# Performance work log

Hardware: AMD Instinct MI355X
Metric: run time of the kernel (lower is better)

The kernel has to match this reference:

```python
import jax, jax.numpy as jnp
import numpy as np
import math

B, L, D, H = 4, 2048, 1024, 16
DK = D // H


def setup_inputs() -> dict:
    key = jax.random.key(0)
    ks = jax.random.split(key, 12)
    scale = math.sqrt(6.0 / (D + D))  # xavier_uniform for square Linear
    def lin(k):
        return jax.random.uniform(k, (D, D), jnp.float32, -scale, scale)
    inp = {
        "query": jax.random.normal(ks[0], (B, L, D), jnp.float32),
        "key": jax.random.normal(ks[1], (B, L, D), jnp.float32),
        "value": jax.random.normal(ks[2], (B, L, D), jnp.float32),
        "Wq": lin(ks[3]), "bq": jnp.zeros((D,), jnp.float32),
        "Wk": lin(ks[4]), "bk": jnp.zeros((D,), jnp.float32),
        "Wv": lin(ks[5]), "bv": jnp.zeros((D,), jnp.float32),
        "Wo": lin(ks[6]), "bo": jnp.zeros((D,), jnp.float32),
        # causal mask: True means masked (hide future positions)
        "attn_mask": jnp.triu(jnp.ones((L, L), dtype=bool), k=1),
    }
    return inp


def reference(query, key, value, Wq, bq, Wk, bk, Wv, bv, Wo, bo, attn_mask):
    def proj(x, W, b):
        # torch Linear: x @ W.T + b ; then split heads -> [B, H, L, DK]
        y = jnp.einsum('bld,ed->ble', x, W) + b
        return y.reshape(B, L, H, DK).transpose(0, 2, 1, 3)

    q = proj(query, Wq, bq)
    k = proj(key, Wk, bk)
    v = proj(value, Wv, bv)

    scores = jnp.einsum('bhqd,bhkd->bhqk', q, k) / jnp.sqrt(jnp.float32(DK))
    scores = jnp.where(attn_mask[None, None, :, :], jnp.float32(-jnp.inf), scores)
    p_attn = jax.nn.softmax(scores, axis=-1)  # dropout p=0 (eval)

    ctx = jnp.einsum('bhqk,bhkd->bhqd', p_attn, v)
    ctx = ctx.transpose(0, 2, 1, 3).reshape(B, L, D)
    out = jnp.einsum('bld,ed->ble', ctx, Wo) + bo
    return out
```

## Files before the change

kernel.cpp:

```cpp
#include <hip/hip_runtime.h>
#include <hip/hip_bf16.h>
#include <stdint.h>

typedef unsigned short u16;
typedef unsigned int u32;
typedef short short8 __attribute__((ext_vector_type(8)));
typedef float f32x4 __attribute__((ext_vector_type(4)));
typedef u32 u32x4 __attribute__((ext_vector_type(4)));
typedef u32 u32x2 __attribute__((ext_vector_type(2)));

#define DEV static __device__ __forceinline__

constexpr int Bsz = 4, Lseq = 2048, Dm = 1024, Hn = 16, Dk = 64;
constexpr float LOG2E = 1.44269504088896340736f;
constexpr float QSCALE = 0.125f * LOG2E;

DEV u16 f2bf(float x) {
    u32 u = __builtin_bit_cast(u32, x);
    return (u16)((u + 0x7fffu + ((u >> 16) & 1u)) >> 16);
}

DEV u32 pk2(float a, float b) {
    __hip_bfloat162 h = __float22bfloat162_rn(float2{a, b});
    u32 r;
    __builtin_memcpy(&r, &h, 4);
    return r;
}

DEV u32x4 ld8_cvt(const float* p) {
    f32x4 lo = *(const f32x4*)p;
    f32x4 hi = *(const f32x4*)(p + 4);
    u32x4 r;
    r[0] = pk2(lo[0], lo[1]);
    r[1] = pk2(lo[2], lo[3]);
    r[2] = pk2(hi[0], hi[1]);
    r[3] = pk2(hi[2], hi[3]);
    return r;
}

DEV void glds16(const void* g, void* l) {
    __builtin_amdgcn_global_load_lds(
        (const __attribute__((address_space(1))) void*)g,
        (__attribute__((address_space(3))) void*)l, 16, 0, 0);
}

__global__ __launch_bounds__(256) void cvt_w3(
    const float* __restrict__ a, const float* __restrict__ b,
    const float* __restrict__ c, u16* __restrict__ d, int n8)
{
    int i = blockIdx.x * 256 + threadIdx.x;
    if (i >= n8) return;
    const float* s = blockIdx.y == 0 ? a : (blockIdx.y == 1 ? b : c);
    ((u32x4*)(d + (size_t)blockIdx.y * (size_t)n8 * 8))[i] = ld8_cvt(s + (long)i * 8);
}

__global__ __launch_bounds__(256) void gemm_oproj(
    const u16* __restrict__ A, const float* __restrict__ W,
    const float* __restrict__ bias, float* __restrict__ Cout)
{
    __shared__ u16 At[2][128 * 32];
    __shared__ u16 Bt[2][128 * 32];

    const int tid = threadIdx.x;
    const int lane = tid & 63, wid = tid >> 6;
    const int wr = wid >> 1, wc = wid & 1;
    const int mbase = blockIdx.x * 128, nbase = blockIdx.y * 128;

    f32x4 acc[4][4];
#pragma unroll
    for (int i = 0; i < 4; i++)
#pragma unroll
        for (int j = 0; j < 4; j++) acc[i][j] = (f32x4)0.f;

    const int srow = lane >> 2;
    const int sseg = (lane & 3) * 8;
    auto stageA = [&](int kt, int buf) {
#pragma unroll
        for (int c = 0; c < 2; c++) {
            const int sec = wid * 2 + c;
            glds16(A + (long)(mbase + sec * 16 + srow) * Dm + (long)kt * 32 + sseg,
                   &At[buf][sec * 512]);
        }
    };

    u32x4 vb[2];
    auto loadB = [&](int kt) {
#pragma unroll
        for (int i = 0; i < 2; i++) {
            int idx = i * 256 + tid;
            int row = idx >> 2, seg = idx & 3;
            vb[i] = ld8_cvt(W + (long)(nbase + row) * Dm + (long)kt * 32 + seg * 8);
        }
    };
    auto writeB = [&](int buf) {
#pragma unroll
        for (int i = 0; i < 2; i++) {
            int idx = i * 256 + tid;
            *(u32x4*)&Bt[buf][idx * 8] = vb[i];
        }
    };

    stageA(0, 0);
    loadB(0);
    writeB(0);
    __syncthreads();

    for (int kt = 0; kt < 32; kt++) {
        const int cur = kt & 1;
        const bool more = (kt + 1 < 32);
        if (more) {
            stageA(kt + 1, cur ^ 1);
            loadB(kt + 1);
        }
        short8 af[4], bfr[4];
#pragma unroll
        for (int mf = 0; mf < 4; mf++)
            af[mf] = *(const short8*)&At[cur][(wr * 64 + mf * 16 + (lane & 15)) * 32 + (lane >> 4) * 8];
#pragma unroll
        for (int nf = 0; nf < 4; nf++)
            bfr[nf] = *(const short8*)&Bt[cur][(wc * 64 + nf * 16 + (lane & 15)) * 32 + (lane >> 4) * 8];
        __builtin_amdgcn_s_setprio(1);
#pragma unroll
        for (int mf = 0; mf < 4; mf++)
#pragma unroll
            for (int nf = 0; nf < 4; nf++)
                acc[mf][nf] = __builtin_amdgcn_mfma_f32_16x16x32_bf16(af[mf], bfr[nf], acc[mf][nf], 0, 0, 0);
        __builtin_amdgcn_s_setprio(0);
        if (more) writeB(cur ^ 1);
        __syncthreads();
    }

#pragma unroll
    for (int nf = 0; nf < 4; nf++) {
        const int n = nbase + wc * 64 + nf * 16 + (lane & 15);
        const float bv = bias[n];
#pragma unroll
        for (int mf = 0; mf < 4; mf++) {
            const int m0 = mbase + wr * 64 + mf * 16 + (lane >> 4) * 4;
#pragma unroll
            for (int r = 0; r < 4; r++) {
                const int m = m0 + r;
                Cout[(long)m * Dm + n] = acc[mf][nf][r] + bv;
            }
        }
    }
}

__global__ __launch_bounds__(256) void gemm_qkv(
    const float* __restrict__ Xq, const float* __restrict__ Xk,
    const float* __restrict__ Xv, const u16* __restrict__ Wb3,
    const float* __restrict__ bq, const float* __restrict__ bk,
    const float* __restrict__ bv, u16* __restrict__ Out3)
{
    __shared__ u16 At[2][128 * 32];
    __shared__ u16 Bt[2][128 * 32];

    const int tid = threadIdx.x;
    const int lane = tid & 63, wid = tid >> 6;
    const int wr = wid >> 1, wc = wid & 1;
    const int mbase = blockIdx.x * 128;
    const int t = blockIdx.y >> 3;
    const int nbase = (blockIdx.y & 7) * 128;
    const float* X = t == 0 ? Xq : (t == 1 ? Xk : Xv);
    const u16* Bw = Wb3 + (size_t)t * Dm * Dm;
    const float* bias = t == 0 ? bq : (t == 1 ? bk : bv);
    const float scale = t == 0 ? QSCALE : 1.0f;
    u16* Cout = Out3 + (size_t)t * ((size_t)Bsz * Lseq * Dm);

    f32x4 acc[4][4];
#pragma unroll
    for (int i = 0; i < 4; i++)
#pragma unroll
        for (int j = 0; j < 4; j++) acc[i][j] = (f32x4)0.f;

    const int srow = lane >> 2;
    const int sseg = (lane & 3) * 8;
    auto stageB = [&](int kt, int buf) {
#pragma unroll
        for (int c = 0; c < 2; c++) {
            const int sec = wid * 2 + c;
            glds16(Bw + (long)(nbase + sec * 16 + srow) * Dm + (long)kt * 32 + sseg,
                   &Bt[buf][sec * 512]);
        }
    };

    u32x4 va[2];
    auto loadA = [&](int kt) {
#pragma unroll
        for (int i = 0; i < 2; i++) {
            int idx = i * 256 + tid;
            int row = idx >> 2, seg = idx & 3;
            va[i] = ld8_cvt(X + (long)(mbase + row) * Dm + (long)kt * 32 + seg * 8);
        }
    };
    auto writeA = [&](int buf) {
#pragma unroll
        for (int i = 0; i < 2; i++) {
            int idx = i * 256 + tid;
            *(u32x4*)&At[buf][idx * 8] = va[i];
        }
    };

    stageB(0, 0);
    loadA(0);
    writeA(0);
    __syncthreads();

    for (int kt = 0; kt < 32; kt++) {
        const int cur = kt & 1;
        const bool more = (kt + 1 < 32);
        if (more) {
            stageB(kt + 1, cur ^ 1);
            loadA(kt + 1);
        }
        short8 af[4], bfr[4];
#pragma unroll
        for (int mf = 0; mf < 4; mf++)
            af[mf] = *(const short8*)&At[cur][(wr * 64 + mf * 16 + (lane & 15)) * 32 + (lane >> 4) * 8];
#pragma unroll
        for (int nf = 0; nf < 4; nf++)
            bfr[nf] = *(const short8*)&Bt[cur][(wc * 64 + nf * 16 + (lane & 15)) * 32 + (lane >> 4) * 8];
        __builtin_amdgcn_s_setprio(1);
#pragma unroll
        for (int mf = 0; mf < 4; mf++)
#pragma unroll
            for (int nf = 0; nf < 4; nf++)
                acc[mf][nf] = __builtin_amdgcn_mfma_f32_16x16x32_bf16(af[mf], bfr[nf], acc[mf][nf], 0, 0, 0);
        __builtin_amdgcn_s_setprio(0);
        if (more) writeA(cur ^ 1);
        __syncthreads();
    }

#pragma unroll
    for (int nf = 0; nf < 4; nf++) {
        const int n = nbase + wc * 64 + nf * 16 + (lane & 15);
        const float bv = bias[n];
#pragma unroll
        for (int mf = 0; mf < 4; mf++) {
            const int m0 = mbase + wr * 64 + mf * 16 + (lane >> 4) * 4;
#pragma unroll
            for (int r = 0; r < 4; r++) {
                const int m = m0 + r;
                const float v = (acc[mf][nf][r] + bv) * scale;
                int b = m >> 11, l = m & 2047, h = n >> 6, dk = n & 63;
                long addr = ((long)(b * Hn + h) * Lseq + l) * Dk + dk;
                Cout[addr] = f2bf(v);
            }
        }
    }
}

__global__ __launch_bounds__(256) void attn_fwd(
    const u16* __restrict__ Qb, const u16* __restrict__ Kb,
    const u16* __restrict__ Vb, u16* __restrict__ Ctx)
{
    __shared__ u16 Kt[2][64 * 64];
    __shared__ u16 Vt[2][64 * 64];
    __shared__ u16 Pq[4][32 * 64];

    const int tid = threadIdx.x, lane = tid & 63, w = tid >> 6;
    const int qt = gridDim.y - 1 - blockIdx.y;
    const int bh = blockIdx.x;
    const long base = (long)bh * Lseq * Dk;
    const int qw = qt * 128 + w * 32;

    const int krow_in_w = lane >> 3;
    const int kseg = lane & 7;
    const int vp = tid >> 3;
    const int vd0 = (tid & 7) * 8;

    auto stage_k = [&](int kvbase, int buf) {
#pragma unroll
        for (int c = 0; c < 2; c++) {
            int kv = w * 16 + c * 8 + krow_in_w;
            int d0 = ((kseg ^ (kv & 7)) * 8);
            glds16(Kb + base + (long)(kvbase + kv) * Dk + d0,
                   &Kt[buf][(w * 16 + c * 8) * 64]);
        }
    };

    auto write_v = [&](int buf, const u32x4& r0, const u32x4& r1) {
        const u16* p0 = (const u16*)&r0;
        const u16* p1 = (const u16*)&r1;
#pragma unroll
        for (int j = 0; j < 8; j++) {
            int d = vd0 + j;
            u32 pr = (u32)p0[j] | ((u32)p1[j] << 16);
            int kvx = (2 * vp) ^ ((((d & 7) ^ (d >> 3)) & 7) << 3);
            *(u32*)&Vt[buf][d * 64 + kvx] = pr;
        }
    };

    short8 qfr[2][2];
#pragma unroll
    for (int qf = 0; qf < 2; qf++)
#pragma unroll
        for (int ks = 0; ks < 2; ks++) {
            int q = qw + qf * 16 + (lane & 15);
            int d0 = ks * 32 + (lane >> 4) * 8;
            qfr[qf][ks] = *(const short8*)(Qb + base + (long)q * Dk + d0);
        }

    f32x4 accT[4][2];
#pragma unroll
    for (int i = 0; i < 4; i++)
#pragma unroll
        for (int j = 0; j < 2; j++) accT[i][j] = (f32x4)0.f;
    float m_run[2] = {-__builtin_inff(), -__builtin_inff()};
    float l_part[2] = {0.f, 0.f};

    u32x4 vr0, vr1;
    stage_k(0, 0);
    vr0 = *(const u32x4*)(Vb + base + (long)(2 * vp) * Dk + vd0);
    vr1 = *(const u32x4*)(Vb + base + (long)(2 * vp + 1) * Dk + vd0);
    write_v(0, vr0, vr1);
    __syncthreads();

    const int nkv = qt * 2 + 2;
    const int myn = ((qw + 31) >> 6) + 1;

    for (int kvt = 0; kvt < nkv; kvt++) {
        const int cur = kvt & 1;
        const bool more = (kvt + 1 < nkv);
        const int kvbase = kvt * 64;

        if (more) {
            stage_k(kvbase + 64, cur ^ 1);
            vr0 = *(const u32x4*)(Vb + base + (long)(kvbase + 64 + 2 * vp) * Dk + vd0);
            vr1 = *(const u32x4*)(Vb + base + (long)(kvbase + 64 + 2 * vp + 1) * Dk + vd0);
        }

        if (kvt < myn) {
            f32x4 st[4][2];
#pragma unroll
            for (int i = 0; i < 4; i++)
#pragma unroll
                for (int j = 0; j < 2; j++) st[i][j] = (f32x4)0.f;
            __builtin_amdgcn_s_setprio(1);
#pragma unroll
            for (int ks = 0; ks < 2; ks++) {
                short8 kf[4];
#pragma unroll
                for (int kvf = 0; kvf < 4; kvf++) {
                    int row = kvf * 16 + (lane & 15);
                    int d0 = ks * 32 + (lane >> 4) * 8;
                    kf[kvf] = *(const short8*)&Kt[cur][row * 64 + (d0 ^ ((row & 7) << 3))];
                }
#pragma unroll
                for (int kvf = 0; kvf < 4; kvf++)
#pragma unroll
                    for (int qf = 0; qf < 2; qf++)
                        st[kvf][qf] = __builtin_amdgcn_mfma_f32_16x16x32_bf16(kf[kvf], qfr[qf][ks], st[kvf][qf], 0, 0, 0);
            }
            __builtin_amdgcn_s_setprio(0);

            if ((kvbase + 63) > qw) {
#pragma unroll
                for (int qf = 0; qf < 2; qf++) {
                    const int q = qw + qf * 16 + (lane & 15);
#pragma unroll
                    for (int kvf = 0; kvf < 4; kvf++)
#pragma unroll
                        for (int r = 0; r < 4; r++) {
                            int kv = kvbase + kvf * 16 + (lane >> 4) * 4 + r;
                            if (kv > q) st[kvf][qf][r] = -1e30f;
                        }
                }
            }

#pragma unroll
            for (int qf = 0; qf < 2; qf++) {
                float tmax = st[0][qf][0];
#pragma unroll
                for (int kvf = 0; kvf < 4; kvf++)
#pragma unroll
                    for (int r = 0; r < 4; r++) tmax = fmaxf(tmax, st[kvf][qf][r]);
                tmax = fmaxf(tmax, __shfl_xor(tmax, 16, 64));
                tmax = fmaxf(tmax, __shfl_xor(tmax, 32, 64));
                const bool norescale = __all((int)(tmax <= m_run[qf] + 8.f));
                if (!norescale) {
                    const float mnew = fmaxf(m_run[qf], tmax);
                    const float sc = __builtin_exp2f(m_run[qf] - mnew);
                    m_run[qf] = mnew;
                    l_part[qf] *= sc;
#pragma unroll
                    for (int dkf = 0; dkf < 4; dkf++)
#pragma unroll
                        for (int r = 0; r < 4; r++) accT[dkf][qf][r] *= sc;
                }
                const float mq = m_run[qf];
                float ts = 0.f;
#pragma unroll
                for (int kvf = 0; kvf < 4; kvf++)
#pragma unroll
                    for (int r = 0; r < 4; r++) {
                        float p = __builtin_exp2f(st[kvf][qf][r] - mq);
                        st[kvf][qf][r] = p;
                        ts += p;
                    }
                l_part[qf] += ts;
                const int qrow = qf * 16 + (lane & 15);
#pragma unroll
                for (int kvf = 0; kvf < 4; kvf++) {
                    u32x2 pk;
                    pk[0] = pk2(st[kvf][qf][0], st[kvf][qf][1]);
                    pk[1] = pk2(st[kvf][qf][2], st[kvf][qf][3]);
                    int kvi = (kvf * 16 + (lane >> 4) * 4) ^ ((lane & 7) << 3);
                    *(u32x2*)&Pq[w][qrow * 64 + kvi] = pk;
                }
            }

#pragma unroll
            for (int kf2 = 0; kf2 < 2; kf2++) {
                short8 vfr[4];
#pragma unroll
                for (int dkf = 0; dkf < 4; dkf++) {
                    int d = dkf * 16 + (lane & 15);
                    int kvi = (kf2 * 32 + (lane >> 4) * 8) ^ ((((d & 7) ^ (d >> 3)) & 7) << 3);
                    vfr[dkf] = *(const short8*)&Vt[cur][d * 64 + kvi];
                }
                short8 pfr[2];
#pragma unroll
                for (int qf = 0; qf < 2; qf++) {
                    int qrow = qf * 16 + (lane & 15);
                    int kvi = (kf2 * 32 + (lane >> 4) * 8) ^ ((lane & 7) << 3);
                    pfr[qf] = *(const short8*)&Pq[w][qrow * 64 + kvi];
                }
                __builtin_amdgcn_s_setprio(1);
#pragma unroll
                for (int dkf = 0; dkf < 4; dkf++)
#pragma unroll
                    for (int qf = 0; qf < 2; qf++)
                        accT[dkf][qf] = __builtin_amdgcn_mfma_f32_16x16x32_bf16(vfr[dkf], pfr[qf], accT[dkf][qf], 0, 0, 0);
                __builtin_amdgcn_s_setprio(0);
            }
        }

        if (more) write_v(cur ^ 1, vr0, vr1);
        __syncthreads();
    }

    const int b = bh >> 4, h = bh & 15;
#pragma unroll
    for (int qf = 0; qf < 2; qf++) {
        float l = l_part[qf];
        l += __shfl_xor(l, 16, 64);
        l += __shfl_xor(l, 32, 64);
        const float inv = 1.f / l;
        const int q = qw + qf * 16 + (lane & 15);
#pragma unroll
        for (int dkf = 0; dkf < 4; dkf++) {
            const int dk0 = dkf * 16 + (lane >> 4) * 4;
            u32x2 o;
            o[0] = pk2(accT[dkf][qf][0] * inv, accT[dkf][qf][1] * inv);
            o[1] = pk2(accT[dkf][qf][2] * inv, accT[dkf][qf][3] * inv);
            long addr = ((long)b * Lseq + q) * Dm + h * Dk + dk0;
            *(u32x2*)(Ctx + addr) = o;
        }
    }
}

extern "C" void kernel_launch(void* const* d_in, const int* in_sizes, int n_in,
                              void* d_out, int out_size, void* d_ws, size_t ws_size,
                              hipStream_t stream)
{
    const float* query = (const float*)d_in[0];
    const float* key_  = (const float*)d_in[1];
    const float* value = (const float*)d_in[2];
    const float* Wq = (const float*)d_in[3];
    const float* bq = (const float*)d_in[4];
    const float* Wk = (const float*)d_in[5];
    const float* bk = (const float*)d_in[6];
    const float* Wv = (const float*)d_in[7];
    const float* bv = (const float*)d_in[8];
    const float* Wo = (const float*)d_in[9];
    const float* bo = (const float*)d_in[10];

    float* out = (float*)d_out;
    const size_t tens = (size_t)Bsz * Lseq * Dm;
    const size_t wTot = (size_t)Dm * Dm;
    u16* Qb = (u16*)d_ws;
    u16* Kb = Qb + tens;
    u16* Vb = Kb + tens;
    u16* Cx = Vb + tens;
    u16* Wqb = Cx;

    dim3 blk(256), g(64, 8), gq(64, 24);
    const int n8w = (int)(wTot / 8);
    const int gw = (n8w + 255) / 256;

    cvt_w3<<<dim3(gw, 3), blk, 0, stream>>>(Wq, Wk, Wv, Wqb, n8w);
    gemm_qkv<<<gq, blk, 0, stream>>>(query, key_, value, Wqb, bq, bk, bv, Qb);
    attn_fwd<<<dim3(Bsz * Hn, Lseq / 128), blk, 0, stream>>>(Qb, Kb, Vb, Cx);
    gemm_oproj<<<g, blk, 0, stream>>>(Cx, Wo, bo, out);
}
```

Before: 212.9 us.

## Switch attention to 32x32x16 MFMA and pass P through registers via permlane swap

The attention kernel moves from 16x16x32 MFMA tiles to 32x32x16 tiles, so each lane owns one query column. The softmax then reduces with a single cross-half shuffle. The probability tile no longer round-trips through shared memory: it is packed to bf16 and rearranged with v_permlane32_swap into the B-operand layout for the PV MFMA. This removes the Pq LDS buffer and its writes and reads, but uses larger accumulator vectors, which raises register pressure and relies on a gfx950-specific instruction.

```diff
diff --git a/kernel.cpp b/kernel.cpp
--- a/kernel.cpp
+++ b/kernel.cpp
@@ -6,6 +6,7 @@
 typedef unsigned int u32;
 typedef short short8 __attribute__((ext_vector_type(8)));
 typedef float f32x4 __attribute__((ext_vector_type(4)));
+typedef float f32x16 __attribute__((ext_vector_type(16)));
 typedef u32 u32x4 __attribute__((ext_vector_type(4)));
 typedef u32 u32x2 __attribute__((ext_vector_type(2)));
 
@@ -42,6 +43,18 @@
     __builtin_amdgcn_global_load_lds(
         (const __attribute__((address_space(1))) void*)g,
         (__attribute__((address_space(3))) void*)l, 16, 0, 0);
+}
+
+DEV void pswap(u32& a, u32& b) {
+    asm volatile("v_permlane32_swap_b32 %0, %1" : "+v"(a), "+v"(b));
+}
+
+DEV short8 mk8(u32 w0, u32 w1, u32 w2, u32 w3) {
+    u32x4 t;
+    t[0] = w0; t[1] = w1; t[2] = w2; t[3] = w3;
+    short8 r;
+    __builtin_memcpy(&r, &t, 16);
+    return r;
 }
 
 __global__ __launch_bounds__(256) void cvt_w3(
@@ -256,13 +269,13 @@
 {
     __shared__ u16 Kt[2][64 * 64];
     __shared__ u16 Vt[2][64 * 64];
-    __shared__ u16 Pq[4][32 * 64];
 
     const int tid = threadIdx.x, lane = tid & 63, w = tid >> 6;
     const int qt = gridDim.y - 1 - blockIdx.y;
     const int bh = blockIdx.x;
     const long base = (long)bh * Lseq * Dk;
     const int qw = qt * 128 + w * 32;
+    const int qcol = lane & 31, hi = lane >> 5;
 
     const int krow_in_w = lane >> 3;
     const int kseg = lane & 7;
@@ -291,23 +304,14 @@
         }
     };
 
-    short8 qfr[2][2];
-#pragma unroll
-    for (int qf = 0; qf < 2; qf++)
-#pragma unroll
-        for (int ks = 0; ks < 2; ks++) {
-            int q = qw + qf * 16 + (lane & 15);
-            int d0 = ks * 32 + (lane >> 4) * 8;
-            qfr[qf][ks] = *(const short8*)(Qb + base + (long)q * Dk + d0);
-        }
-
-    f32x4 accT[4][2];
-#pragma unroll
-    for (int i = 0; i < 4; i++)
-#pragma unroll
-        for (int j = 0; j < 2; j++) accT[i][j] = (f32x4)0.f;
-    float m_run[2] = {-__builtin_inff(), -__builtin_inff()};
-    float l_part[2] = {0.f, 0.f};
+    short8 qfr[4];
+#pragma unroll
+    for (int ks = 0; ks < 4; ks++)
+        qfr[ks] = *(const short8*)(Qb + base + (long)(qw + qcol) * Dk + ks * 16 + hi * 8);
+
+    f32x16 acc0 = (f32x16)0.f, acc1 = (f32x16)0.f;
+    float m_run = -__builtin_inff();
+    float l_part = 0.f;
 
     u32x4 vr0, vr1;
     stage_k(0, 0);
@@ -331,131 +335,136 @@
         }
 
         if (kvt < myn) {
-            f32x4 st[4][2];
-#pragma unroll
-            for (int i = 0; i < 4; i++)
-#pragma unroll
-                for (int j = 0; j < 2; j++) st[i][j] = (f32x4)0.f;
+            f32x16 st0 = (f32x16)0.f, st1 = (f32x16)0.f;
             __builtin_amdgcn_s_setprio(1);
 #pragma unroll
-            for (int ks = 0; ks < 2; ks++) {
-                short8 kf[4];
-#pragma unroll
-                for (int kvf = 0; kvf < 4; kvf++) {
-                    int row = kvf * 16 + (lane & 15);
-                    int d0 = ks * 32 + (lane >> 4) * 8;
-                    kf[kvf] = *(const short8*)&Kt[cur][row * 64 + (d0 ^ ((row & 7) << 3))];
+            for (int ks = 0; ks < 4; ks++) {
+                const int d0 = ks * 16 + hi * 8;
+                {
+                    const int kvrow = qcol;
+                    short8 kf = *(const short8*)&Kt[cur][kvrow * 64 + (d0 ^ ((kvrow & 7) << 3))];
+                    st0 = __builtin_amdgcn_mfma_f32_32x32x16_bf16(kf, qfr[ks], st0, 0, 0, 0);
                 }
-#pragma unroll
-                for (int kvf = 0; kvf < 4; kvf++)
-#pragma unroll
-                    for (int qf = 0; qf < 2; qf++)
-                        st[kvf][qf] = __builtin_amdgcn_mfma_f32_16x16x32_bf16(kf[kvf], qfr[qf][ks], st[kvf][qf], 0, 0, 0);
+                {
+                    const int kvrow = 32 + qcol;
+                    short8 kf = *(const short8*)&Kt[cur][kvrow * 64 + (d0 ^ ((kvrow & 7) << 3))];
+                    st1 = __builtin_amdgcn_mfma_f32_32x32x16_bf16(kf, qfr[ks], st1, 0, 0, 0);
+                }
             }
             __builtin_amdgcn_s_setprio(0);
 
             if ((kvbase + 63) > qw) {
-#pragma unroll
-                for (int qf = 0; qf < 2; qf++) {
-                    const int q = qw + qf * 16 + (lane & 15);
-#pragma unroll
-                    for (int kvf = 0; kvf < 4; kvf++)
-#pragma unroll
-                        for (int r = 0; r < 4; r++) {
-                            int kv = kvbase + kvf * 16 + (lane >> 4) * 4 + r;
-                            if (kv > q) st[kvf][qf][r] = -1e30f;
-                        }
+                const int q = qw + qcol;
+#pragma unroll
+                for (int r = 0; r < 16; r++) {
+                    const int rr = (r & 3) + 8 * (r >> 2) + 4 * hi;
+                    if (kvbase + rr > q) st0[r] = -1e30f;
+                    if (kvbase + 32 + rr > q) st1[r] = -1e30f;
                 }
             }
 
-#pragma unroll
-            for (int qf = 0; qf < 2; qf++) {
-                float tmax = st[0][qf][0];
-#pragma unroll
-                for (int kvf = 0; kvf < 4; kvf++)
-#pragma unroll
-                    for (int r = 0; r < 4; r++) tmax = fmaxf(tmax, st[kvf][qf][r]);
-                tmax = fmaxf(tmax, __shfl_xor(tmax, 16, 64));
-                tmax = fmaxf(tmax, __shfl_xor(tmax, 32, 64));
-                const bool norescale = __all((int)(tmax <= m_run[qf] + 8.f));
-                if (!norescale) {
-                    const float mnew = fmaxf(m_run[qf], tmax);
-                    const float sc = __builtin_exp2f(m_run[qf] - mnew);
-                    m_run[qf] = mnew;
-                    l_part[qf] *= sc;
-#pragma unroll
-                    for (int dkf = 0; dkf < 4; dkf++)
-#pragma unroll
-                        for (int r = 0; r < 4; r++) accT[dkf][qf][r] *= sc;
+            float tmax = st0[0];
+#pragma unroll
+            for (int r = 1; r < 16; r++) tmax = fmaxf(tmax, st0[r]);
+#pragma unroll
+            for (int r = 0; r < 16; r++) tmax = fmaxf(tmax, st1[r]);
+            tmax = fmaxf(tmax, __shfl_xor(tmax, 32, 64));
+            const bool norescale = __all((int)(tmax <= m_run + 8.f));
+            if (!norescale) {
+                const float mnew = fmaxf(m_run, tmax);
+                const float sc = __builtin_exp2f(m_run - mnew);
+                m_run = mnew;
+                l_part *= sc;
+#pragma unroll
+                for (int r = 0; r < 16; r++) {
+                    acc0[r] *= sc;
+                    acc1[r] *= sc;
                 }
-                const float mq = m_run[qf];
-                float ts = 0.f;
-#pragma unroll
-                for (int kvf = 0; kvf < 4; kvf++)
-#pragma unroll
-                    for (int r = 0; r < 4; r++) {
-                        float p = __builtin_exp2f(st[kvf][qf][r] - mq);
-                        st[kvf][qf][r] = p;
-                        ts += p;
-                    }
-                l_part[qf] += ts;
-                const int qrow = qf * 16 + (lane & 15);
-#pragma unroll
-                for (int kvf = 0; kvf < 4; kvf++) {
-                    u32x2 pk;
-                    pk[0] = pk2(st[kvf][qf][0], st[kvf][qf][1]);
-                    pk[1] = pk2(st[kvf][qf][2], st[kvf][qf][3]);
-                    int kvi = (kvf * 16 + (lane >> 4) * 4) ^ ((lane & 7) << 3);
-                    *(u32x2*)&Pq[w][qrow * 64 + kvi] = pk;
+            }
+            float ts = 0.f;
+#pragma unroll
+            for (int r = 0; r < 16; r++) {
+                float p = __builtin_exp2f(st0[r] - m_run);
+                st0[r] = p;
+                ts += p;
+            }
+#pragma unroll
+            for (int r = 0; r < 16; r++) {
+                float p = __builtin_exp2f(st1[r] - m_run);
+                st1[r] = p;
+                ts += p;
+            }
+            l_part += ts;
+
+            short8 pf[4];
+            {
+                u32 a0 = pk2(st0[0], st0[1]), a1 = pk2(st0[2], st0[3]);
+                u32 b0 = pk2(st0[4], st0[5]), b1 = pk2(st0[6], st0[7]);
+                pswap(a0, b0);
+                pswap(a1, b1);
+                pf[0] = mk8(a0, a1, b0, b1);
+                u32 c0 = pk2(st0[8], st0[9]), c1 = pk2(st0[10], st0[11]);
+                u32 e0 = pk2(st0[12], st0[13]), e1 = pk2(st0[14], st0[15]);
+                pswap(c0, e0);
+                pswap(c1, e1);
+                pf[1] = mk8(c0, c1, e0, e1);
+            }
+            {
+                u32 a0 = pk2(st1[0], st1[1]), a1 = pk2(st1[2], st1[3]);
+                u32 b0 = pk2(st1[4], st1[5]), b1 = pk2(st1[6], st1[7]);
+                pswap(a0, b0);
+                pswap(a1, b1);
+                pf[2] = mk8(a0, a1, b0, b1);
+                u32 c0 = pk2(st1[8], st1[9]), c1 = pk2(st1[10], st1[11]);
+                u32 e0 = pk2(st1[12], st1[13]), e1 = pk2(st1[14], st1[15]);
+                pswap(c0, e0);
+                pswap(c1, e1);
+                pf[3] = mk8(c0, c1, e0, e1);
+            }
+
+            __builtin_amdgcn_s_setprio(1);
+#pragma unroll
+            for (int s = 0; s < 4; s++) {
+                {
+                    const int d = qcol;
+                    const int kvi = (s * 16 + hi * 8) ^ ((((d & 7) ^ (d >> 3)) & 7) << 3);
+                    short8 vf = *(const short8*)&Vt[cur][d * 64 + kvi];
+                    acc0 = __builtin_amdgcn_mfma_f32_32x32x16_bf16(vf, pf[s], acc0, 0, 0, 0);
                 }
-            }
-
-#pragma unroll
-            for (int kf2 = 0; kf2 < 2; kf2++) {
-                short8 vfr[4];
-#pragma unroll
-                for (int dkf = 0; dkf < 4; dkf++) {
-                    int d = dkf * 16 + (lane & 15);
-                    int kvi = (kf2 * 32 + (lane >> 4) * 8) ^ ((((d & 7) ^ (d >> 3)) & 7) << 3);
-                    vfr[dkf] = *(const short8*)&Vt[cur][d * 64 + kvi];
+                {
+                    const int d = 32 + qcol;
+                    const int kvi = (s * 16 + hi * 8) ^ ((((d & 7) ^ (d >> 3)) & 7) << 3);
+                    short8 vf = *(const short8*)&Vt[cur][d * 64 + kvi];
+                    acc1 = __builtin_amdgcn_mfma_f32_32x32x16_bf16(vf, pf[s], acc1, 0, 0, 0);
                 }
-                short8 pfr[2];
-#pragma unroll
-                for (int qf = 0; qf < 2; qf++) {
-                    int qrow = qf * 16 + (lane & 15);
-                    int kvi = (kf2 * 32 + (lane >> 4) * 8) ^ ((lane & 7) << 3);
-                    pfr[qf] = *(const short8*)&Pq[w][qrow * 64 + kvi];
-                }
-                __builtin_amdgcn_s_setprio(1);
-#pragma unroll
-                for (int dkf = 0; dkf < 4; dkf++)
-#pragma unroll
-                    for (int qf = 0; qf < 2; qf++)
-                        accT[dkf][qf] = __builtin_amdgcn_mfma_f32_16x16x32_bf16(vfr[dkf], pfr[qf], accT[dkf][qf], 0, 0, 0);
-                __builtin_amdgcn_s_setprio(0);
-            }
+            }
+            __builtin_amdgcn_s_setprio(0);
         }
 
         if (more) write_v(cur ^ 1, vr0, vr1);
         __syncthreads();
     }
 
-    const int b = bh >> 4, h = bh & 15;
-#pragma unroll
-    for (int qf = 0; qf < 2; qf++) {
-        float l = l_part[qf];
-        l += __shfl_xor(l, 16, 64);
-        l += __shfl_xor(l, 32, 64);
-        const float inv = 1.f / l;
-        const int q = qw + qf * 16 + (lane & 15);
-#pragma unroll
-        for (int dkf = 0; dkf < 4; dkf++) {
-            const int dk0 = dkf * 16 + (lane >> 4) * 4;
+    const int b = bh >> 4, hh = bh & 15;
+    float l = l_part + __shfl_xor(l_part, 32, 64);
+    const float inv = 1.f / l;
+    const int q = qw + qcol;
+    const long rowaddr = ((long)b * Lseq + q) * Dm + hh * Dk;
+#pragma unroll
+    for (int quad = 0; quad < 4; quad++) {
+        {
+            const int dk0 = quad * 8 + 4 * hi;
             u32x2 o;
-            o[0] = pk2(accT[dkf][qf][0] * inv, accT[dkf][qf][1] * inv);
-            o[1] = pk2(accT[dkf][qf][2] * inv, accT[dkf][qf][3] * inv);
-            long addr = ((long)b * Lseq + q) * Dm + h * Dk + dk0;
-            *(u32x2*)(Ctx + addr) = o;
+            o[0] = pk2(acc0[quad * 4 + 0] * inv, acc0[quad * 4 + 1] * inv);
+            o[1] = pk2(acc0[quad * 4 + 2] * inv, acc0[quad * 4 + 3] * inv);
+            *(u32x2*)(Ctx + rowaddr + dk0) = o;
+        }
+        {
+            const int dk0 = 32 + quad * 8 + 4 * hi;
+            u32x2 o;
+            o[0] = pk2(acc1[quad * 4 + 0] * inv, acc1[quad * 4 + 1] * inv);
+            o[1] = pk2(acc1[quad * 4 + 2] * inv, acc1[quad * 4 + 3] * inv);
+            *(u32x2*)(Ctx + rowaddr + dk0) = o;
         }
     }
 }
```

Result: no change. 210.1 us, median of 3 (-1.3%).
